# Optimization experiments

Hardware: AMD Instinct MI355X
Metric: run time of the kernel (lower is better)

The kernel has to match this reference:

```python
import jax, jax.numpy as jnp
import numpy as np

T = 4096          # timesteps per modality
D_QK = 64
D = D_QK + 2      # feature dim incl. timestamp channel = 66
M = 4             # number of modalities
N_LIN = 3         # n_layers=2 hidden layers -> 3 Linear layers in the MLP


def setup_inputs() -> dict:
    key = jax.random.key(0)
    ks = jax.random.split(key, 2 * M + 2)
    inp = {}
    for m in range(M):
        feats = jax.random.normal(ks[2 * m], (1, 1, T, D - 1), dtype=jnp.float32)
        # last feature channel is a sorted event timestamp, as the source reads X[0,0,:,-1]
        ts = jnp.sort(jax.random.uniform(ks[2 * m + 1], (T,), dtype=jnp.float32))
        inp[f"x{m + 1}"] = jnp.concatenate([feats, ts[None, None, :, None]], axis=-1)
    scale = 1.0 / np.sqrt(D).astype(np.float32)
    inp["wq"] = jax.random.normal(ks[2 * M], (N_LIN, D, D), dtype=jnp.float32) * scale
    inp["bq"] = jnp.zeros((N_LIN, D), dtype=jnp.float32)
    inp["wk"] = jax.random.normal(ks[2 * M + 1], (N_LIN, D, D), dtype=jnp.float32) * scale
    inp["bk"] = jnp.zeros((N_LIN, D), dtype=jnp.float32)
    return inp


def _mlp(x, W, b):
    # MLP(d, [d]*2, d, relu): relu after hidden linears, none after the last
    h = x
    for i in range(N_LIN - 1):
        h = jax.nn.relu(h @ W[i] + b[i])
    return h @ W[N_LIN - 1] + b[N_LIN - 1]


def _causal_dot_product(Q, K, V, t1, t2):
    """Cross-modality causal linear attention with timestamps.
    Q:(T1,d) queries at times t1; K:(T2,d), V:(T2,dv) at times t2 (sorted).
    out[i] = Q[i] @ sum_{j : t2[j] <= t1[i]} K[j] (x) V[j]
    Implemented as a cumulative outer-product state + gather (scan form).
    """
    state = jnp.cumsum(K[:, :, None] * V[:, None, :], axis=0)   # (T2, d, dv)
    idx = jnp.searchsorted(t2, t1, side="right") - 1            # last key with t2 <= t1[i]
    S = state[jnp.clip(idx, 0)]                                  # (T1, d, dv)
    S = jnp.where((idx >= 0)[:, None, None], S, jnp.zeros_like(S))
    return jnp.einsum("td,tdv->tv", Q, S)                        # (T1, dv)


def reference(x1, x2, x3, x4, wq, bq, wk, bk):
    xs = [x1, x2, x3, x4]
    Q = _mlp(x1, wq, bq)[0, 0]      # (T1, D)
    t1 = x1[0, 0, :, -1]
    outs = []
    for xm in xs:                   # fixed small loop over M modalities
        Km = _mlp(xm, wk, bk)[0, 0]  # shared W_K[0], as in the source
        Vm = xm[0, 0]                # V = X
        t2 = xm[0, 0, :, -1]
        outs.append(_causal_dot_product(Q, Km, Vm, t1, t2))
    Z = jnp.stack(outs, axis=0)     # (M, T1, D) == Zout[0]
    yhat = Z.sum(0)[None, :, :2]    # (1, T1, 2)
    return yhat
```

## Files before the change

### kernel.cpp

```cpp
#include <hip/hip_runtime.h>

#define T 4096
#define D 66
#define NL 3
#define NC 64
#define JC 64
#define DD (D * D)
#define HSB 104
#define KTS 68

typedef short bf16x8 __attribute__((ext_vector_type(8)));
typedef float f32x4  __attribute__((ext_vector_type(4)));

__device__ __forceinline__ unsigned short f2bf(float f) {
    unsigned int u = __builtin_bit_cast(unsigned int, f);
    u += 0x7fff + ((u >> 16) & 1);
    return (unsigned short)(u >> 16);
}
__device__ __forceinline__ float bf2f(unsigned short b) {
    return __builtin_bit_cast(float, (unsigned int)b << 16);
}

__global__ __launch_bounds__(256) void mlp_scan_kernel(
    const float* __restrict__ x1, const float* __restrict__ x2,
    const float* __restrict__ x3, const float* __restrict__ x4,
    const float* __restrict__ wq, const float* __restrict__ bq,
    const float* __restrict__ wk, const float* __restrict__ bk,
    float* __restrict__ Q, unsigned short* __restrict__ Sb,
    float* __restrict__ chunkSum, float* __restrict__ TM)
{
    __shared__ short Hs[64 * HSB];
    __shared__ short Wt[80 * HSB];
    __shared__ float KT[D * KTS];
    __shared__ float side[3][64];

    const int t    = threadIdx.x;
    const bool isQ = blockIdx.x >= 256;
    const int m    = isQ ? 0 : (blockIdx.x >> 6);
    const int j0   = (isQ ? (blockIdx.x - 256) : (blockIdx.x & 63)) * 64;
    const float* X  = (isQ || m == 0) ? x1 : (m == 1 ? x2 : (m == 2 ? x3 : x4));
    const float* W  = isQ ? wq : wk;
    const float* Bs = isQ ? bq : bk;

    const float2* xt2 = (const float2*)(X + (size_t)j0 * D);
    for (int k = t; k < 64 * 33; k += 256) {
        const int r  = k / 33;
        const int dp = (k - r * 33) * 2;
        const float2 v = xt2[k];
        Hs[r * HSB + dp]     = f2bf(v.x);
        Hs[r * HSB + dp + 1] = f2bf(v.y);
        if (dp == 0)  { side[0][r] = v.x; side[1][r] = v.y; }
        if (dp == 64) { side[2][r] = v.y; }
    }
    for (int k = t; k < 64 * (HSB - D); k += 256) {
        const int r = k / (HSB - D);
        const int d = D + (k - r * (HSB - D));
        Hs[r * HSB + d] = 0;
    }
    {
        int* wz = (int*)Wt;
        for (int k = t; k < 80 * HSB / 2; k += 256) wz[k] = 0;
    }

    float wreg[18];
#pragma unroll
    for (int i = 0; i < 18; ++i) {
        const int k = t + i * 256;
        if (k < DD) wreg[i] = W[k];
    }

    const int lane = t & 63;
    const int wv   = t >> 6;
    const int lrow = lane & 15;
    const int kg   = (lane >> 4) * 8;
    const int cr0  = (lane >> 4) * 4;

    __syncthreads();

#pragma unroll 1
    for (int l = 0; l < NL; ++l) {
#pragma unroll
        for (int i = 0; i < 18; ++i) {
            const int k = t + i * 256;
            if (k < DD) {
                const int kk = k / D;
                const int o  = k - kk * D;
                Wt[o * HSB + kk] = f2bf(wreg[i]);
            }
        }
        __syncthreads();

        if (l < NL - 1) {
            const float* Wg = W + (l + 1) * DD;
#pragma unroll
            for (int i = 0; i < 18; ++i) {
                const int k = t + i * 256;
                if (k < DD) wreg[i] = Wg[k];
            }
        }

        const int abase = (wv * 16 + lrow) * HSB + kg;
        const bf16x8 a0 = *(const bf16x8*)&Hs[abase];
        const bf16x8 a1 = *(const bf16x8*)&Hs[abase + 32];
        const bf16x8 a2 = *(const bf16x8*)&Hs[abase + 64];

        f32x4 acc[5];
#pragma unroll
        for (int nt = 0; nt < 5; ++nt) {
            const short* wb = &Wt[(nt * 16 + lrow) * HSB + kg];
            f32x4 c = {0.0f, 0.0f, 0.0f, 0.0f};
            c = __builtin_amdgcn_mfma_f32_16x16x32_bf16(a0, *(const bf16x8*)(wb),      c, 0, 0, 0);
            c = __builtin_amdgcn_mfma_f32_16x16x32_bf16(a1, *(const bf16x8*)(wb + 32), c, 0, 0, 0);
            c = __builtin_amdgcn_mfma_f32_16x16x32_bf16(a2, *(const bf16x8*)(wb + 64), c, 0, 0, 0);
            acc[nt] = c;
        }
        __syncthreads();

#pragma unroll
        for (int nt = 0; nt < 5; ++nt) {
            const int col = nt * 16 + lrow;
            const float bias = (col < D) ? Bs[l * D + col] : 0.0f;
#pragma unroll
            for (int r = 0; r < 4; ++r) {
                const int row = wv * 16 + cr0 + r;
                float v = acc[nt][r] + bias;
                if (l < NL - 1) {
                    v = fmaxf(v, 0.0f);
                    Hs[row * HSB + col] = f2bf(v);
                } else if (isQ) {
                    if (col < D) Q[(size_t)(j0 + row) * D + col] = v;
                } else {
                    if (col < D) KT[col * KTS + row] = v;
                }
            }
        }
    }

    __syncthreads();

    if (!isQ) {
        const int c = t;
        if (c >= 144 && c < 144 + JC) TM[m * T + j0 + (c - 144)] = side[2][c - 144];
        if (c < 132) {
            const int d = c >> 1;
            const int v = c & 1;
            float run = 0.0f;
#pragma unroll 8
            for (int jj = 0; jj < JC; ++jj) {
                run = fmaf(KT[d * KTS + jj], side[v][jj], run);
                Sb[((size_t)m * T + j0 + jj) * 132 + c] = f2bf(run);
            }
            chunkSum[((size_t)m * NC + j0 / JC) * 132 + c] = run;
        }
    }
}

__global__ __launch_bounds__(256) void chunkscan_kernel(
    const float* __restrict__ chunkSum, float* __restrict__ chunkOff)
{
    const int wv   = threadIdx.x >> 6;
    const int lane = threadIdx.x & 63;
    const int c    = blockIdx.x * 4 + wv;
    const int m    = blockIdx.y;
    if (c >= 132) return;

    const float v = chunkSum[((size_t)m * NC + lane) * 132 + c];
    float inc = v;
#pragma unroll
    for (int off = 1; off < 64; off <<= 1) {
        const float y = __shfl_up(inc, off);
        if (lane >= off) inc += y;
    }
    chunkOff[((size_t)m * NC + lane) * 132 + c] = inc - v;
}

__global__ __launch_bounds__(256) void out_kernel(
    const float* __restrict__ Q, const unsigned short* __restrict__ Sb,
    const float* __restrict__ chunkOff, const float* __restrict__ TM,
    float* __restrict__ out)
{
    __shared__ float segEnd[4][64];
    const int w    = threadIdx.x >> 6;
    const int lane = threadIdx.x & 63;
    const int i    = blockIdx.x * 4 + w;

    segEnd[w][lane] = TM[w * T + lane * 64 + 63];
    const float t1i = TM[i];
    const float q0  = Q[(size_t)i * D + lane];
    const float q1  = (lane < 2) ? Q[(size_t)i * D + 64 + lane] : 0.0f;
    float acc0 = 0.0f, acc1 = 0.0f;
    __syncthreads();

    int seg[4];
#pragma unroll
    for (int mm = 0; mm < 4; ++mm) {
        const unsigned long long b = __ballot(segEnd[mm][lane] <= t1i);
        const int hi = __popcll(b);
        seg[mm] = (hi < 63) ? hi : 63;
    }
    int idx[4];
#pragma unroll
    for (int mm = 0; mm < 4; ++mm) {
        const float sv = TM[mm * T + seg[mm] * 64 + lane];
        const unsigned long long b = __ballot(sv <= t1i);
        idx[mm] = seg[mm] * 64 + __popcll(b) - 1;
    }

#pragma unroll
    for (int mm = 0; mm < 4; ++mm) {
        if (idx[mm] >= 0) {
            const unsigned short* sp = Sb + ((size_t)mm * T + idx[mm]) * 132;
            const float* op = chunkOff + ((size_t)mm * NC + (idx[mm] / JC)) * 132;
            const ushort2 s0 = *(const ushort2*)(sp + lane * 2);
            const float2  c0 = *(const float2*)(op + lane * 2);
            acc0 = fmaf(q0, bf2f(s0.x) + c0.x, acc0);
            acc1 = fmaf(q0, bf2f(s0.y) + c0.y, acc1);
            if (lane < 2) {
                const ushort2 s1 = *(const ushort2*)(sp + 128 + lane * 2);
                const float2  c1 = *(const float2*)(op + 128 + lane * 2);
                acc0 = fmaf(q1, bf2f(s1.x) + c1.x, acc0);
                acc1 = fmaf(q1, bf2f(s1.y) + c1.y, acc1);
            }
        }
    }

#pragma unroll
    for (int off = 32; off >= 1; off >>= 1) {
        acc0 += __shfl_down(acc0, off);
        acc1 += __shfl_down(acc1, off);
    }
    if (lane == 0) {
        out[(size_t)i * 2 + 0] = acc0;
        out[(size_t)i * 2 + 1] = acc1;
    }
}

extern "C" void kernel_launch(void* const* d_in, const int* in_sizes, int n_in,
                              void* d_out, int out_size, void* d_ws, size_t ws_size,
                              hipStream_t stream)
{
    (void)in_sizes; (void)n_in; (void)out_size; (void)ws_size;
    const float* x1 = (const float*)d_in[0];
    const float* x2 = (const float*)d_in[1];
    const float* x3 = (const float*)d_in[2];
    const float* x4 = (const float*)d_in[3];
    const float* wq = (const float*)d_in[4];
    const float* bq = (const float*)d_in[5];
    const float* wk = (const float*)d_in[6];
    const float* bk = (const float*)d_in[7];

    float* ws = (float*)d_ws;
    float*          Q        = ws;
    unsigned short* Sb       = (unsigned short*)(ws + 270336);
    float*          chunkSum = ws + 1351680;
    float*          chunkOff = ws + 1385472;
    float*          TM       = ws + 1419264;

    mlp_scan_kernel<<<320, 256, 0, stream>>>(x1, x2, x3, x4, wq, bq, wk, bk,
                                             Q, Sb, chunkSum, TM);
    chunkscan_kernel<<<dim3(33, 4), 256, 0, stream>>>(chunkSum, chunkOff);
    out_kernel<<<1024, 256, 0, stream>>>(Q, Sb, chunkOff, TM, (float*)d_out);
}
```

Baseline: 27.82 us.

## Fuse chunk prefix scan into output kernel with atomic-counter grid sync

```diff
diff --git a/kernel.cpp b/kernel.cpp
--- a/kernel.cpp
+++ b/kernel.cpp
@@ -7,7 +7,8 @@
 #define JC 64
 #define DD (D * D)
 #define HSB 104
-#define KTS 68
+#define KTS 67
+#define NPROD 132
 
 typedef short bf16x8 __attribute__((ext_vector_type(8)));
 typedef float f32x4  __attribute__((ext_vector_type(4)));
@@ -19,6 +20,17 @@
 }
 __device__ __forceinline__ float bf2f(unsigned short b) {
     return __builtin_bit_cast(float, (unsigned int)b << 16);
+}
+
+__device__ __forceinline__ void st_sc(float* p, float v) {
+    asm volatile("global_store_dword %0, %1, off sc0 sc1" :: "v"(p), "v"(v));
+}
+__device__ __forceinline__ int coherent_poll(const int* p) {
+    int v;
+    asm volatile("global_load_dword %0, %1, off sc0 sc1\n\t"
+                 "s_waitcnt vmcnt(0)"
+                 : "=v"(v) : "v"(p) : "memory");
+    return v;
 }
 
 __global__ __launch_bounds__(256) void mlp_scan_kernel(
@@ -57,9 +69,13 @@
         const int d = D + (k - r * (HSB - D));
         Hs[r * HSB + d] = 0;
     }
-    {
-        int* wz = (int*)Wt;
-        for (int k = t; k < 80 * HSB / 2; k += 256) wz[k] = 0;
+    for (int k = t; k < 80 * 19; k += 256) {
+        const int r = k / 19;
+        ((int*)&Wt[r * HSB + 66])[k - r * 19] = 0;
+    }
+    for (int k = t; k < 14 * 33; k += 256) {
+        const int r = k / 33;
+        ((int*)&Wt[(66 + r) * HSB])[k - r * 33] = 0;
     }
 
     float wreg[18];
@@ -155,28 +171,10 @@
     }
 }
 
-__global__ __launch_bounds__(256) void chunkscan_kernel(
-    const float* __restrict__ chunkSum, float* __restrict__ chunkOff)
-{
-    const int wv   = threadIdx.x >> 6;
-    const int lane = threadIdx.x & 63;
-    const int c    = blockIdx.x * 4 + wv;
-    const int m    = blockIdx.y;
-    if (c >= 132) return;
-
-    const float v = chunkSum[((size_t)m * NC + lane) * 132 + c];
-    float inc = v;
-#pragma unroll
-    for (int off = 1; off < 64; off <<= 1) {
-        const float y = __shfl_up(inc, off);
-        if (lane >= off) inc += y;
-    }
-    chunkOff[((size_t)m * NC + lane) * 132 + c] = inc - v;
-}
-
 __global__ __launch_bounds__(256) void out_kernel(
     const float* __restrict__ Q, const unsigned short* __restrict__ Sb,
-    const float* __restrict__ chunkOff, const float* __restrict__ TM,
+    const float* __restrict__ chunkSum, float* __restrict__ chunkOff,
+    const float* __restrict__ TM, int* __restrict__ done,
     float* __restrict__ out)
 {
     __shared__ float segEnd[4][64];
@@ -184,13 +182,35 @@
     const int lane = threadIdx.x & 63;
     const int i    = blockIdx.x * 4 + w;
 
+    if (blockIdx.x < NPROD) {
+        const int m = blockIdx.x & 3;
+        const int c = (blockIdx.x >> 2) * 4 + w;
+        const float v = chunkSum[((size_t)m * NC + lane) * 132 + c];
+        float inc = v;
+#pragma unroll
+        for (int off = 1; off < 64; off <<= 1) {
+            const float y = __shfl_up(inc, off);
+            if (lane >= off) inc += y;
+        }
+        st_sc(chunkOff + ((size_t)m * NC + lane) * 132 + c, inc - v);
+        asm volatile("s_waitcnt vmcnt(0)" ::: "memory");
+        __syncthreads();
+        if (threadIdx.x == 0)
+            __hip_atomic_fetch_add(done, 1, __ATOMIC_RELAXED, __HIP_MEMORY_SCOPE_AGENT);
+    }
+
     segEnd[w][lane] = TM[w * T + lane * 64 + 63];
     const float t1i = TM[i];
     const float q0  = Q[(size_t)i * D + lane];
     const float q1  = (lane < 2) ? Q[(size_t)i * D + 64 + lane] : 0.0f;
+
+    if (threadIdx.x == 0) {
+        while (coherent_poll(done) < NPROD)
+            __builtin_amdgcn_s_sleep(2);
+    }
+    __syncthreads();
+
     float acc0 = 0.0f, acc1 = 0.0f;
-    __syncthreads();
-
     int seg[4];
 #pragma unroll
     for (int mm = 0; mm < 4; ++mm) {
@@ -255,9 +275,12 @@
     float*          chunkSum = ws + 1351680;
     float*          chunkOff = ws + 1385472;
     float*          TM       = ws + 1419264;
+    int*            done     = (int*)(ws + 1435648);
+
+    hipMemsetAsync(done, 0, sizeof(int), stream);
 
     mlp_scan_kernel<<<320, 256, 0, stream>>>(x1, x2, x3, x4, wq, bq, wk, bk,
                                              Q, Sb, chunkSum, TM);
-    chunkscan_kernel<<<dim3(33, 4), 256, 0, stream>>>(chunkSum, chunkOff);
-    out_kernel<<<1024, 256, 0, stream>>>(Q, Sb, chunkOff, TM, (float*)d_out);
-}
+    out_kernel<<<1024, 256, 0, stream>>>(Q, Sb, chunkSum, chunkOff, TM, done,
+                                         (float*)d_out);
+}
```

New measurement: 44.17 us. 58.8% more time.
